# Kernel tuning notes

Measured on AMD Instinct MI355X. Metric: run time of the kernel, lower is better.

## Reference

```python
import jax, jax.numpy as jnp
import numpy as np

DM = 1024
N_HEADS = 16
DK = DM // N_HEADS
BS, SEQ = 4, 2048


def setup_inputs() -> dict:
    key = jax.random.key(0)
    k1, k2, k3 = jax.random.split(key, 3)
    scale = 1.0 / np.sqrt(DM)
    return {
        "x": jax.random.normal(k1, (BS, SEQ, DM), dtype=jnp.float32),
        "w_qkv": jax.random.normal(k2, (DM, 3 * DM), dtype=jnp.float32) * scale,
        "b_qkv": jnp.zeros((3 * DM,), dtype=jnp.float32),
        "w_out": jax.random.normal(k3, (DM, DM), dtype=jnp.float32) * scale,
        "b_out": jnp.zeros((DM,), dtype=jnp.float32),
    }


def reference(x, w_qkv, b_qkv, w_out, b_out):
    bs, seq_len, dm = x.shape
    qkv = x @ w_qkv + b_qkv                      # [bs, seq, 3*dm]
    q, k, v = jnp.split(qkv, 3, axis=-1)
    # [bs, heads, seq, dk]
    def heads(t):
        return t.reshape(bs, seq_len, N_HEADS, DK).transpose(0, 2, 1, 3)
    q, k, v = heads(q), heads(k), heads(v)
    w = jnp.einsum("bhqd,bhkd->bhqk", q, k) / np.sqrt(DK)
    causal = jnp.tril(jnp.ones((seq_len, seq_len), dtype=bool))
    w = jnp.where(causal, w, -jnp.inf)
    w = jax.nn.softmax(w, axis=-1)               # attn_dropout p=0 -> identity
    z = jnp.einsum("bhqk,bhkd->bhqd", w, v)
    z = z.transpose(0, 2, 1, 3).reshape(bs, seq_len, dm)
    return z @ w_out + b_out                     # resid_dropout p=0 -> identity
```

## Files before the change

kernel.cpp:

```cpp
#include <hip/hip_runtime.h>
#include <hip/hip_bf16.h>

typedef unsigned short u16;
typedef unsigned int u32;
typedef short bf16x8 __attribute__((ext_vector_type(8)));
typedef float f32x4 __attribute__((ext_vector_type(4)));

#define DM 1024
#define SEQ 2048
#define MTOK 8192
#define NQKV 3072

#define QSCALE 0.18033688011112042f

#define BAR() __builtin_amdgcn_s_barrier()
#define VMW(n) asm volatile("s_waitcnt vmcnt(" #n ")" ::: "memory")
#define LGKW() asm volatile("s_waitcnt lgkmcnt(0)" ::: "memory")

__device__ __forceinline__ u16 f2bf(float f) {
  union { float f; unsigned u; } a; a.f = f;
  unsigned r = a.u + 0x7FFFu + ((a.u >> 16) & 1u);
  return (u16)(r >> 16);
}

__device__ __forceinline__ u32 cvt2(float a, float b) {
  __hip_bfloat162 t = __float22bfloat162_rn(make_float2(a, b));
  u32 r; __builtin_memcpy(&r, &t, 4); return r;
}

__device__ __forceinline__ void gload_lds16(const u16* g, u16* l) {
  __builtin_amdgcn_global_load_lds(
      (const __attribute__((address_space(1))) unsigned int*)g,
      (__attribute__((address_space(3))) unsigned int*)l, 16, 0, 0);
}

__global__ __launch_bounds__(256) void cast_x_kernel(const float* __restrict__ in,
                                                     u16* __restrict__ out) {
  int i = blockIdx.x * 256 + threadIdx.x;
  float4 v = ((const float4*)in)[i];
  ushort4 o;
  o.x = f2bf(v.x); o.y = f2bf(v.y); o.z = f2bf(v.z); o.w = f2bf(v.w);
  ((ushort4*)out)[i] = o;
}

__global__ __launch_bounds__(256) void transpose_cast_kernel(const float* __restrict__ in,
                                                             u16* __restrict__ out,
                                                             int R, int C) {
  __shared__ float tile[32][33];
  const int tx = threadIdx.x & 31, ty = threadIdx.x >> 5;
  const int r0 = blockIdx.y << 5, c0 = blockIdx.x << 5;
#pragma unroll
  for (int i = 0; i < 32; i += 8)
    tile[ty + i][tx] = in[(size_t)(r0 + ty + i) * C + (c0 + tx)];
  __syncthreads();
#pragma unroll
  for (int i = 0; i < 32; i += 8)
    out[(size_t)(c0 + ty + i) * R + (r0 + tx)] = f2bf(tile[tx][ty + i]);
}

__global__ __launch_bounds__(256) void fill_vpad_kernel(u16* __restrict__ vT) {
  const int i = blockIdx.x * 256 + threadIdx.x;
  const int col4 = i & (SEQ / 4 - 1);
  const int rowg = i >> 9;
  const int bh = rowg >> 4, r = rowg & 15;
  const u16 val = (r == 0) ? (u16)0x3F80 : (u16)0;
  ushort4 o; o.x = val; o.y = val; o.z = val; o.w = val;
  ((ushort4*)(vT + ((size_t)bh * 80 + 64 + r) * SEQ))[col4] = o;
}

template <int EPI>
__global__ __launch_bounds__(256, 2) void gemm2_kernel(
    const u16* __restrict__ A, const u16* __restrict__ Bt,
    const float* __restrict__ bias,
    u16* __restrict__ oq, u16* __restrict__ ok, u16* __restrict__ ovT,
    float* __restrict__ of, int N) {
  __shared__ alignas(16) u16 As[2][128 * 64];
  __shared__ alignas(16) u16 Bs[2][128 * 64];

  const int tid = threadIdx.x, lane = tid & 63, wid = tid >> 6;
  const int wr = wid >> 1, wc = wid & 1;
  const int l15 = lane & 15, l4 = lane >> 4;
  const int swz = l15 & 7;

  const int xcd = blockIdx.x & 7, idx = blockIdx.x >> 3;
  const int row0 = ((xcd << 3) + (idx & 7)) << 7;
  const int col0 = (idx >> 3) << 7;

  const int sr = tid >> 3;
  const int scsw = ((tid & 7) ^ (sr & 7)) << 3;
  const u16* asrc = A + (size_t)(row0 + sr) * 1024 + scsw;
  const u16* bsrc = Bt + (size_t)(col0 + sr) * 1024 + scsw;

  auto stage = [&](int buf, int kt) {
#pragma unroll
    for (int j = 0; j < 4; ++j)
      gload_lds16(asrc + (size_t)(j << 5) * 1024 + (kt << 6),
                  &As[buf][0] + (j << 11) + tid * 8);
#pragma unroll
    for (int j = 0; j < 4; ++j)
      gload_lds16(bsrc + (size_t)(j << 5) * 1024 + (kt << 6),
                  &Bs[buf][0] + (j << 11) + tid * 8);
  };

  f32x4 acc[4][4];
#pragma unroll
  for (int m = 0; m < 4; ++m)
#pragma unroll
    for (int n = 0; n < 4; ++n) acc[m][n] = (f32x4){0.f, 0.f, 0.f, 0.f};

  stage(0, 0);
  stage(1, 1);

  int cur = 0;
#pragma unroll 1
  for (int t = 0; t < 16; ++t) {
    if (t < 15) { VMW(8); } else { VMW(0); }
    BAR();

    bf16x8 af[4][2], bfr[4][2];
    {
      const u16* base = &As[cur][0] + ((wr << 6) + l15) * 64;
#pragma unroll
      for (int mf = 0; mf < 4; ++mf)
#pragma unroll
        for (int ks = 0; ks < 2; ++ks)
          af[mf][ks] = *(const bf16x8*)(base + (mf << 4) * 64 + ((((ks << 2) + l4) ^ swz) << 3));
    }
    {
      const u16* base = &Bs[cur][0] + ((wc << 6) + l15) * 64;
#pragma unroll
      for (int nf = 0; nf < 4; ++nf)
#pragma unroll
        for (int ks = 0; ks < 2; ++ks)
          bfr[nf][ks] = *(const bf16x8*)(base + (nf << 4) * 64 + ((((ks << 2) + l4) ^ swz) << 3));
    }
    LGKW();
    BAR();
    if (t < 14) stage(cur, t + 2);

    __builtin_amdgcn_s_setprio(1);
#pragma unroll
    for (int ks = 0; ks < 2; ++ks)
#pragma unroll
      for (int mf = 0; mf < 4; ++mf)
#pragma unroll
        for (int nf = 0; nf < 4; ++nf)
          acc[mf][nf] = __builtin_amdgcn_mfma_f32_16x16x32_bf16(af[mf][ks], bfr[nf][ks],
                                                                acc[mf][nf], 0, 0, 0);
    __builtin_amdgcn_s_setprio(0);
    cur ^= 1;
  }

#pragma unroll
  for (int nf = 0; nf < 4; ++nf) {
    const int col = col0 + (wc << 6) + (nf << 4) + l15;
    const float bv = bias[col];
    if (EPI == 0) {
      const int sel = col >> 10;
      const int h = (col & 1023) >> 6;
      const int d = col & 63;
      const float scl = (sel == 0) ? QSCALE : 1.0f;
#pragma unroll
      for (int mf = 0; mf < 4; ++mf)
#pragma unroll
        for (int r = 0; r < 4; ++r) {
          const int row = row0 + (wr << 6) + (mf << 4) + (l4 << 2) + r;
          const int bb = row >> 11, s = row & 2047;
          const u16 v = f2bf((acc[mf][nf][r] + bv) * scl);
          const int bh = (bb << 4) + h;
          if (sel == 0)      oq[((size_t)bh * SEQ + s) * 64 + d] = v;
          else if (sel == 1) ok[((size_t)bh * SEQ + s) * 64 + d] = v;
          else               ovT[((size_t)bh * 80 + d) * SEQ + s] = v;
        }
    } else {
#pragma unroll
      for (int mf = 0; mf < 4; ++mf)
#pragma unroll
        for (int r = 0; r < 4; ++r) {
          const int row = row0 + (wr << 6) + (mf << 4) + (l4 << 2) + r;
          of[(size_t)row * N + col] = acc[mf][nf][r] + bv;
        }
    }
  }
}

__global__ __launch_bounds__(512, 4) void attn_kernel(const u16* __restrict__ qb,
                                                      const u16* __restrict__ kbuf,
                                                      const u16* __restrict__ vT,
                                                      u16* __restrict__ zb) {
  __shared__ alignas(16) u16 Ks[2][64 * 64];
  __shared__ alignas(16) u16 Vs[2][80 * 64];
  __shared__ alignas(16) u16 Ps[8][32 * 64];

  const int bid = blockIdx.x;
  const int xcd = bid & 7;
  const int idx = bid >> 3;
  const int bh = (xcd << 3) | (idx & 7);
  const int qpart = idx >> 3;
  const int qseg = (qpart < 4) ? (7 - qpart) : (qpart - 4);
  const int b = bh >> 4, h = bh & 15;

  const int tid = threadIdx.x;
  const int lane = tid & 63, wid = tid >> 6;
  const int l15 = lane & 15, l4 = lane >> 4;
  const int swz = l15 & 7;

  const u16* qp = qb + (size_t)bh * SEQ * 64;
  const u16* kp = kbuf + (size_t)bh * SEQ * 64;
  const u16* vp = vT + (size_t)bh * 80 * SEQ;

  const int qw0 = qseg * 256 + (wid << 5);
  const int nkt = (qseg + 1) << 2;
  const int ktmax = (qseg << 2) + (wid >> 1);

  const int srow = tid >> 3, schk = tid & 7;
  const u16* ksrc  = kp + (size_t)srow * 64 + ((schk ^ (srow & 7)) << 3);
  const u16* vsrc  = vp + (size_t)srow * SEQ + ((schk ^ (srow & 7)) << 3);
  const u16* vsrc2 = vp + (size_t)(64 + srow) * SEQ + ((schk ^ (srow & 7)) << 3);

  auto stage = [&](int buf, int kt) {
    gload_lds16(ksrc + (size_t)kt * 4096, &Ks[buf][0] + tid * 8);
    gload_lds16(vsrc + (size_t)kt * 64, &Vs[buf][0] + tid * 8);
    if (tid < 128) gload_lds16(vsrc2 + (size_t)kt * 64, &Vs[buf][0] + 4096 + tid * 8);
  };

  bf16x8 aq[2][2];
#pragma unroll
  for (int m = 0; m < 2; ++m)
#pragma unroll
    for (int c = 0; c < 2; ++c)
      aq[m][c] = *(const bf16x8*)(qp + (size_t)(qw0 + (m << 4) + l15) * 64 + (c << 5) + (l4 << 3));

  f32x4 zo[2][5];
  float mrun[2] = {-INFINITY, -INFINITY};
#pragma unroll
  for (int m = 0; m < 2; ++m)
#pragma unroll
    for (int d = 0; d < 5; ++d) zo[m][d] = (f32x4){0.f, 0.f, 0.f, 0.f};

  u16* pw = &Ps[wid][0];

  stage(0, 0);
  __syncthreads();

  int cur = 0;
  for (int kt = 0; kt < nkt; ++kt) {
    if (kt + 1 < nkt) stage(cur ^ 1, kt + 1);

    if (kt <= ktmax) {
      const int k0 = kt << 6;
      const u16* kb_ = &Ks[cur][0];
      const u16* vb_ = &Vs[cur][0];
      f32x4 s[2][4];
#pragma unroll
      for (int m = 0; m < 2; ++m)
#pragma unroll
        for (int nf = 0; nf < 4; ++nf) s[m][nf] = (f32x4){0.f, 0.f, 0.f, 0.f};
#pragma unroll
      for (int nf = 0; nf < 4; ++nf) {
        const u16* kr = kb_ + ((nf << 4) + l15) * 64;
        const bf16x8 kf0 = *(const bf16x8*)(kr + ((l4 ^ swz) << 3));
        const bf16x8 kf1 = *(const bf16x8*)(kr + (((l4 + 4) ^ swz) << 3));
#pragma unroll
        for (int m = 0; m < 2; ++m) {
          s[m][nf] = __builtin_amdgcn_mfma_f32_16x16x32_bf16(kf0, aq[m][0], s[m][nf], 0, 0, 0);
          s[m][nf] = __builtin_amdgcn_mfma_f32_16x16x32_bf16(kf1, aq[m][1], s[m][nf], 0, 0, 0);
        }
      }
      if (kt == ktmax) {
#pragma unroll
        for (int m = 0; m < 2; ++m) {
          const int qtok = qw0 + (m << 4) + l15;
#pragma unroll
          for (int nf = 0; nf < 4; ++nf)
#pragma unroll
            for (int r = 0; r < 4; ++r) {
              const int ktok = k0 + (nf << 4) + (l4 << 2) + r;
              if (ktok > qtok) s[m][nf][r] = -INFINITY;
            }
        }
      }
#pragma unroll
      for (int m = 0; m < 2; ++m) {
        float mx = s[m][0][0];
#pragma unroll
        for (int nf = 0; nf < 4; ++nf)
#pragma unroll
          for (int r = 0; r < 4; ++r) mx = fmaxf(mx, s[m][nf][r]);
        mx = fmaxf(mx, __shfl_xor(mx, 16));
        mx = fmaxf(mx, __shfl_xor(mx, 32));
        if (__ballot(mx > mrun[m])) {
          const float mnew = fmaxf(mrun[m], mx);
          const float alpha = exp2f(mrun[m] - mnew);
          mrun[m] = mnew;
#pragma unroll
          for (int d = 0; d < 5; ++d) zo[m][d] *= alpha;
        }
        const int row = (m << 4) + l15;
#pragma unroll
        for (int nf = 0; nf < 4; ++nf) {
          f32x4 p;
#pragma unroll
          for (int r = 0; r < 4; ++r) p[r] = exp2f(s[m][nf][r] - mrun[m]);
          const int phys = ((nf << 1) + (l4 >> 1)) ^ swz;
          uint2 o; o.x = cvt2(p[0], p[1]); o.y = cvt2(p[2], p[3]);
          *(u32*)(pw + row * 64 + phys * 8 + ((l4 & 1) << 2)) = o.x;
          *(u32*)(pw + row * 64 + phys * 8 + ((l4 & 1) << 2) + 2) = o.y;
        }
      }
      bf16x8 pa[2][2];
#pragma unroll
      for (int m = 0; m < 2; ++m)
#pragma unroll
        for (int c = 0; c < 2; ++c) {
          const int phys = ((c << 2) + l4) ^ swz;
          pa[m][c] = *(const bf16x8*)(pw + ((m << 4) + l15) * 64 + phys * 8);
        }
#pragma unroll
      for (int d = 0; d < 5; ++d) {
        const u16* vr = vb_ + ((d << 4) + l15) * 64;
        const bf16x8 vf0 = *(const bf16x8*)(vr + ((l4 ^ swz) << 3));
        const bf16x8 vf1 = *(const bf16x8*)(vr + (((l4 + 4) ^ swz) << 3));
        zo[0][d] = __builtin_amdgcn_mfma_f32_16x16x32_bf16(vf0, pa[0][0], zo[0][d], 0, 0, 0);
        zo[0][d] = __builtin_amdgcn_mfma_f32_16x16x32_bf16(vf1, pa[0][1], zo[0][d], 0, 0, 0);
        zo[1][d] = __builtin_amdgcn_mfma_f32_16x16x32_bf16(vf0, pa[1][0], zo[1][d], 0, 0, 0);
        zo[1][d] = __builtin_amdgcn_mfma_f32_16x16x32_bf16(vf1, pa[1][1], zo[1][d], 0, 0, 0);
      }
    }
    __syncthreads();
    cur ^= 1;
  }

#pragma unroll
  for (int m = 0; m < 2; ++m) {
    const float sm = __shfl(zo[m][4][0], l15);
    const float inv = 1.0f / sm;
    const int q = qw0 + (m << 4) + l15;
#pragma unroll
    for (int d = 0; d < 4; ++d) {
      uint2 o;
      o.x = cvt2(zo[m][d][0] * inv, zo[m][d][1] * inv);
      o.y = cvt2(zo[m][d][2] * inv, zo[m][d][3] * inv);
      *(uint2*)(zb + (((size_t)b * SEQ + q) * 16 + h) * 64 + (d << 4) + (l4 << 2)) = o;
    }
  }
}

extern "C" void kernel_launch(void* const* d_in, const int* in_sizes, int n_in,
                              void* d_out, int out_size, void* d_ws, size_t ws_size,
                              hipStream_t stream) {
  const float* x     = (const float*)d_in[0];
  const float* w_qkv = (const float*)d_in[1];
  const float* b_qkv = (const float*)d_in[2];
  const float* w_out = (const float*)d_in[3];
  const float* b_out = (const float*)d_in[4];
  float* out = (float*)d_out;

  char* ws = (char*)d_ws;
  u16* xb    = (u16*)ws;  ws += (size_t)MTOK * DM * 2;
  u16* wqkvT = (u16*)ws;  ws += (size_t)NQKV * DM * 2;
  u16* woutT = (u16*)ws;  ws += (size_t)DM * DM * 2;
  u16* qb    = (u16*)ws;  ws += (size_t)MTOK * DM * 2;
  u16* kb    = (u16*)ws;  ws += (size_t)MTOK * DM * 2;
  u16* vTb   = (u16*)ws;  ws += (size_t)64 * 80 * SEQ * 2;
  u16* zbuf  = (u16*)ws;  ws += (size_t)MTOK * DM * 2;

  cast_x_kernel<<<MTOK * DM / 1024, 256, 0, stream>>>(x, xb);
  transpose_cast_kernel<<<dim3(NQKV / 32, DM / 32), 256, 0, stream>>>(w_qkv, wqkvT, DM, NQKV);
  transpose_cast_kernel<<<dim3(DM / 32, DM / 32), 256, 0, stream>>>(w_out, woutT, DM, DM);
  fill_vpad_kernel<<<2048, 256, 0, stream>>>(vTb);

  gemm2_kernel<0><<<1536, 256, 0, stream>>>(xb, wqkvT, b_qkv, qb, kb, vTb, nullptr, NQKV);

  attn_kernel<<<512, 512, 0, stream>>>(qb, kb, vTb, zbuf);

  gemm2_kernel<1><<<512, 256, 0, stream>>>(zbuf, woutT, b_out, nullptr, nullptr, nullptr, out, DM);
}
```

Measured before the change: 199.5 us.

## Drop padded V rows, compute row sums with ones MFMA, deepen K/V prefetch

The V^T buffer no longer carries 16 padding rows (a ones row plus zeros) used to get the softmax row sum through the PV MFMA. The sum now comes from MFMAs against an in-register ones fragment, which removes the fill kernel and shrinks V staging and LDS. The attention loop also changes from one-ahead staging with two syncthreads to issuing loads two tiles ahead, gated by vmcnt waits and raw barriers. This gives more load/compute overlap, but correctness now depends on the waitcnt accounting being right.

```diff
diff --git a/kernel.cpp b/kernel.cpp
--- a/kernel.cpp
+++ b/kernel.cpp
@@ -56,16 +56,6 @@
 #pragma unroll
   for (int i = 0; i < 32; i += 8)
     out[(size_t)(c0 + ty + i) * R + (r0 + tx)] = f2bf(tile[tx][ty + i]);
-}
-
-__global__ __launch_bounds__(256) void fill_vpad_kernel(u16* __restrict__ vT) {
-  const int i = blockIdx.x * 256 + threadIdx.x;
-  const int col4 = i & (SEQ / 4 - 1);
-  const int rowg = i >> 9;
-  const int bh = rowg >> 4, r = rowg & 15;
-  const u16 val = (r == 0) ? (u16)0x3F80 : (u16)0;
-  ushort4 o; o.x = val; o.y = val; o.z = val; o.w = val;
-  ((ushort4*)(vT + ((size_t)bh * 80 + 64 + r) * SEQ))[col4] = o;
 }
 
 template <int EPI>
@@ -170,7 +160,7 @@
           const int bh = (bb << 4) + h;
           if (sel == 0)      oq[((size_t)bh * SEQ + s) * 64 + d] = v;
           else if (sel == 1) ok[((size_t)bh * SEQ + s) * 64 + d] = v;
-          else               ovT[((size_t)bh * 80 + d) * SEQ + s] = v;
+          else               ovT[((size_t)bh * 64 + d) * SEQ + s] = v;
         }
     } else {
 #pragma unroll
@@ -189,7 +179,7 @@
                                                       const u16* __restrict__ vT,
                                                       u16* __restrict__ zb) {
   __shared__ alignas(16) u16 Ks[2][64 * 64];
-  __shared__ alignas(16) u16 Vs[2][80 * 64];
+  __shared__ alignas(16) u16 Vs[2][64 * 64];
   __shared__ alignas(16) u16 Ps[8][32 * 64];
 
   const int bid = blockIdx.x;
@@ -207,21 +197,20 @@
 
   const u16* qp = qb + (size_t)bh * SEQ * 64;
   const u16* kp = kbuf + (size_t)bh * SEQ * 64;
-  const u16* vp = vT + (size_t)bh * 80 * SEQ;
+  const u16* vp = vT + (size_t)bh * 64 * SEQ;
 
   const int qw0 = qseg * 256 + (wid << 5);
   const int nkt = (qseg + 1) << 2;
   const int ktmax = (qseg << 2) + (wid >> 1);
 
-  const int srow = tid >> 3, schk = tid & 7;
-  const u16* ksrc  = kp + (size_t)srow * 64 + ((schk ^ (srow & 7)) << 3);
-  const u16* vsrc  = vp + (size_t)srow * SEQ + ((schk ^ (srow & 7)) << 3);
-  const u16* vsrc2 = vp + (size_t)(64 + srow) * SEQ + ((schk ^ (srow & 7)) << 3);
+  const int srow = tid >> 3;
+  const int schk = ((tid & 7) ^ (srow & 7)) << 3;
+  const u16* ksrc = kp + (size_t)srow * 64 + schk;
+  const u16* vsrc = vp + (size_t)srow * SEQ + schk;
 
   auto stage = [&](int buf, int kt) {
     gload_lds16(ksrc + (size_t)kt * 4096, &Ks[buf][0] + tid * 8);
     gload_lds16(vsrc + (size_t)kt * 64, &Vs[buf][0] + tid * 8);
-    if (tid < 128) gload_lds16(vsrc2 + (size_t)kt * 64, &Vs[buf][0] + 4096 + tid * 8);
   };
 
   bf16x8 aq[2][2];
@@ -230,6 +219,10 @@
 #pragma unroll
     for (int c = 0; c < 2; ++c)
       aq[m][c] = *(const bf16x8*)(qp + (size_t)(qw0 + (m << 4) + l15) * 64 + (c << 5) + (l4 << 3));
+  asm volatile("" :: "v"(aq[0][0]), "v"(aq[0][1]), "v"(aq[1][0]), "v"(aq[1][1]));
+
+  const short osv = (short)0x3F80;
+  const bf16x8 onesf = {osv, osv, osv, osv, osv, osv, osv, osv};
 
   f32x4 zo[2][5];
   float mrun[2] = {-INFINITY, -INFINITY};
@@ -241,11 +234,13 @@
   u16* pw = &Ps[wid][0];
 
   stage(0, 0);
-  __syncthreads();
+  stage(1, 1);
 
   int cur = 0;
+#pragma unroll 1
   for (int kt = 0; kt < nkt; ++kt) {
-    if (kt + 1 < nkt) stage(cur ^ 1, kt + 1);
+    if (kt + 1 < nkt) { VMW(2); } else { VMW(0); }
+    BAR();
 
     if (kt <= ktmax) {
       const int k0 = kt << 6;
@@ -303,9 +298,8 @@
 #pragma unroll
           for (int r = 0; r < 4; ++r) p[r] = exp2f(s[m][nf][r] - mrun[m]);
           const int phys = ((nf << 1) + (l4 >> 1)) ^ swz;
-          uint2 o; o.x = cvt2(p[0], p[1]); o.y = cvt2(p[2], p[3]);
-          *(u32*)(pw + row * 64 + phys * 8 + ((l4 & 1) << 2)) = o.x;
-          *(u32*)(pw + row * 64 + phys * 8 + ((l4 & 1) << 2) + 2) = o.y;
+          *(u32*)(pw + row * 64 + phys * 8 + ((l4 & 1) << 2)) = cvt2(p[0], p[1]);
+          *(u32*)(pw + row * 64 + phys * 8 + ((l4 & 1) << 2) + 2) = cvt2(p[2], p[3]);
         }
       }
       bf16x8 pa[2][2];
@@ -317,7 +311,7 @@
           pa[m][c] = *(const bf16x8*)(pw + ((m << 4) + l15) * 64 + phys * 8);
         }
 #pragma unroll
-      for (int d = 0; d < 5; ++d) {
+      for (int d = 0; d < 4; ++d) {
         const u16* vr = vb_ + ((d << 4) + l15) * 64;
         const bf16x8 vf0 = *(const bf16x8*)(vr + ((l4 ^ swz) << 3));
         const bf16x8 vf1 = *(const bf16x8*)(vr + (((l4 + 4) ^ swz) << 3));
@@ -326,15 +320,20 @@
         zo[1][d] = __builtin_amdgcn_mfma_f32_16x16x32_bf16(vf0, pa[1][0], zo[1][d], 0, 0, 0);
         zo[1][d] = __builtin_amdgcn_mfma_f32_16x16x32_bf16(vf1, pa[1][1], zo[1][d], 0, 0, 0);
       }
-    }
-    __syncthreads();
+      zo[0][4] = __builtin_amdgcn_mfma_f32_16x16x32_bf16(onesf, pa[0][0], zo[0][4], 0, 0, 0);
+      zo[0][4] = __builtin_amdgcn_mfma_f32_16x16x32_bf16(onesf, pa[0][1], zo[0][4], 0, 0, 0);
+      zo[1][4] = __builtin_amdgcn_mfma_f32_16x16x32_bf16(onesf, pa[1][0], zo[1][4], 0, 0, 0);
+      zo[1][4] = __builtin_amdgcn_mfma_f32_16x16x32_bf16(onesf, pa[1][1], zo[1][4], 0, 0, 0);
+    }
+
+    BAR();
+    if (kt + 2 < nkt) stage(cur, kt + 2);
     cur ^= 1;
   }
 
 #pragma unroll
   for (int m = 0; m < 2; ++m) {
-    const float sm = __shfl(zo[m][4][0], l15);
-    const float inv = 1.0f / sm;
+    const float inv = 1.0f / zo[m][4][0];
     const int q = qw0 + (m << 4) + l15;
 #pragma unroll
     for (int d = 0; d < 4; ++d) {
@@ -362,13 +361,12 @@
   u16* woutT = (u16*)ws;  ws += (size_t)DM * DM * 2;
   u16* qb    = (u16*)ws;  ws += (size_t)MTOK * DM * 2;
   u16* kb    = (u16*)ws;  ws += (size_t)MTOK * DM * 2;
-  u16* vTb   = (u16*)ws;  ws += (size_t)64 * 80 * SEQ * 2;
+  u16* vTb   = (u16*)ws;  ws += (size_t)MTOK * DM * 2;
   u16* zbuf  = (u16*)ws;  ws += (size_t)MTOK * DM * 2;
 
   cast_x_kernel<<<MTOK * DM / 1024, 256, 0, stream>>>(x, xb);
   transpose_cast_kernel<<<dim3(NQKV / 32, DM / 32), 256, 0, stream>>>(w_qkv, wqkvT, DM, NQKV);
   transpose_cast_kernel<<<dim3(DM / 32, DM / 32), 256, 0, stream>>>(w_out, woutT, DM, DM);
-  fill_vpad_kernel<<<2048, 256, 0, stream>>>(vTb);
 
   gemm2_kernel<0><<<1536, 256, 0, stream>>>(xb, wqkvT, b_qkv, qb, kb, vTb, nullptr, NQKV);
 
```

After: 202.3 us. About the same (+1.4%).
